# Optimization experiments

Hardware: AMD Instinct MI355X
Metric: run time of the kernel (lower is better)

The kernel has to match this reference:

```python
import jax, jax.numpy as jnp
import numpy as np

HIDDEN = 4096
NUM_HEADS = 32
NUM_KV_HEADS = 8
HEAD_DIM = HIDDEN // NUM_HEADS  # 128
ROPE_THETA = 10000.0
T = 2048


def setup_inputs() -> dict:
    key = jax.random.key(0)
    k1, k2, k3 = jax.random.split(key, 3)
    positions = jnp.arange(T, dtype=jnp.int32)
    hidden_states = jax.random.normal(k1, (T, HIDDEN), dtype=jnp.float32)
    # 0.02 init scale keeps logits in a sane range
    Wqkv = jax.random.normal(k2, (HIDDEN, (NUM_HEADS + 2 * NUM_KV_HEADS) * HEAD_DIM), dtype=jnp.float32) * 0.02
    Wo = jax.random.normal(k3, (HIDDEN, HIDDEN), dtype=jnp.float32) * 0.02
    return {"positions": positions, "hidden_states": hidden_states, "Wqkv": Wqkv, "Wo": Wo}


def _rope_neox(x, positions):
    # x: [T, H, D]; neox style rotates halves of the head dim
    d2 = HEAD_DIM // 2
    inv_freq = ROPE_THETA ** (-jnp.arange(0, d2, dtype=jnp.float32) / d2)
    ang = positions.astype(jnp.float32)[:, None] * inv_freq  # [T, d2]
    cos = jnp.cos(ang)[:, None, :]  # [T,1,d2]
    sin = jnp.sin(ang)[:, None, :]
    x1, x2 = x[..., :d2], x[..., d2:]
    return jnp.concatenate([x1 * cos - x2 * sin, x2 * cos + x1 * sin], axis=-1)


def reference(positions, hidden_states, Wqkv, Wo):
    Tn = hidden_states.shape[0]
    q_sz = NUM_HEADS * HEAD_DIM
    kv_sz = NUM_KV_HEADS * HEAD_DIM
    qkv = hidden_states @ Wqkv  # [T, q_sz + 2*kv_sz]
    q = qkv[:, :q_sz].reshape(Tn, NUM_HEADS, HEAD_DIM)
    k = qkv[:, q_sz:q_sz + kv_sz].reshape(Tn, NUM_KV_HEADS, HEAD_DIM)
    v = qkv[:, q_sz + kv_sz:].reshape(Tn, NUM_KV_HEADS, HEAD_DIM)
    q = _rope_neox(q, positions)
    k = _rope_neox(k, positions)
    # GQA: repeat kv heads to match q heads
    rep = NUM_HEADS // NUM_KV_HEADS
    k = jnp.repeat(k, rep, axis=1)  # [T, H, D]
    v = jnp.repeat(v, rep, axis=1)
    scale = HEAD_DIM ** -0.5
    scores = jnp.einsum('thd,shd->hts', q, k) * scale  # [H, T, T]
    causal = positions[:, None] >= positions[None, :]  # [T, T]
    scores = jnp.where(causal[None, :, :], scores, jnp.float32(-1e30))
    probs = jax.nn.softmax(scores, axis=-1)
    attn = jnp.einsum('hts,shd->thd', probs, v).reshape(Tn, HIDDEN)
    return attn @ Wo
```

## Files before the change

### kernel.cpp

```cpp
#include <hip/hip_runtime.h>
#include <hip/hip_bf16.h>
#include <math.h>

#define T_SEQ 2048
#define HID   4096
#define NH    32
#define NKV   8
#define HD    128
#define QKVD  6144
#define KOFF  4096
#define VOFF  5120

typedef unsigned short u16;
typedef unsigned int   u32;
typedef __attribute__((ext_vector_type(4))) float f32x4;
typedef __attribute__((ext_vector_type(8))) short s16x8;
typedef __attribute__((ext_vector_type(4))) unsigned short u16x4;

__device__ inline u16 f2bf(float f) {
  u32 u = __float_as_uint(f);
  u32 r = u + 0x7FFFu + ((u >> 16) & 1u);
  return (u16)(r >> 16);
}
__device__ inline float bf2f(u16 h) { return __uint_as_float(((u32)h) << 16); }

__device__ inline void gl_lds16(const void* g, void* l) {
  __builtin_amdgcn_global_load_lds((const __attribute__((address_space(1))) void*)g,
                                   (__attribute__((address_space(3))) void*)l, 16, 0, 0);
}

__global__ void cast_f32_bf16(const float* __restrict__ in, u16* __restrict__ out, int n) {
  int i = (blockIdx.x * blockDim.x + threadIdx.x) * 4;
  if (i < n) {
    float4 v = *(const float4*)(in + i);
    u16x4 o = { f2bf(v.x), f2bf(v.y), f2bf(v.z), f2bf(v.w) };
    *(u16x4*)(out + i) = o;
  }
}

__global__ void transpose_cast(const float* __restrict__ in, u16* __restrict__ out, int K, int N) {
  __shared__ float tile[32][33];
  int n0 = blockIdx.x * 32, k0 = blockIdx.y * 32;
  int tx = threadIdx.x, ty = threadIdx.y;
  for (int i = ty; i < 32; i += 8)
    tile[i][tx] = in[(size_t)(k0 + i) * N + n0 + tx];
  __syncthreads();
  for (int i = ty; i < 32; i += 8)
    out[(size_t)(n0 + i) * K + k0 + tx] = f2bf(tile[tx][i]);
}

__global__ void vtrans(const u16* __restrict__ qkv, u16* __restrict__ Vt) {
  __shared__ u16 tile[32][33];
  int kv = blockIdx.z;
  int t0 = blockIdx.x * 32, d0 = blockIdx.y * 32;
  int tx = threadIdx.x, ty = threadIdx.y;
  for (int i = ty; i < 32; i += 8)
    tile[i][tx] = qkv[(size_t)(t0 + i) * QKVD + VOFF + kv * HD + d0 + tx];
  __syncthreads();
  for (int i = ty; i < 32; i += 8)
    Vt[(size_t)(kv * HD + d0 + i) * T_SEQ + t0 + tx] = tile[tx][i];
}

__global__ void rope_kernel(u16* __restrict__ qkv, const int* __restrict__ positions) {
  int t = blockIdx.x;
  int h = blockIdx.y * 4 + (threadIdx.x >> 6);
  int i = threadIdx.x & 63;
  float pos = (float)positions[t];
  float freq = exp2f(-(float)i * (13.287712379549449f / 64.0f));
  float ang = pos * freq;
  float s, c;
  sincosf(ang, &s, &c);
  size_t off;
  if (h < NH) off = (size_t)t * QKVD + h * HD;
  else        off = (size_t)t * QKVD + KOFF + (h - NH) * HD;
  float x1 = bf2f(qkv[off + i]);
  float x2 = bf2f(qkv[off + 64 + i]);
  qkv[off + i]      = f2bf(x1 * c - x2 * s);
  qkv[off + 64 + i] = f2bf(x2 * c + x1 * s);
}

__device__ inline void stage_unit(const u16* __restrict__ G, int K, u16* lds, int w, int l) {
  const int rl = l >> 3;
  const int row = 8 * w + rl;
  const int cs = ((l & 7) ^ rl) << 3;
  gl_lds16(G + (size_t)row * K + cs, lds + 8 * w * 64);
}

#define RD(base, row) (*(const s16x8*)((base) + (size_t)(row) * 64 + ((((kk) * 4 + lg) ^ xsw) << 3)))
#define MM(i, j) acc[i][j] = __builtin_amdgcn_mfma_f32_16x16x32_bf16(a[i][kk], b[j][kk], acc[i][j], 0, 0, 0)

__global__ __launch_bounds__(512, 2) void gemm_qkv(const u16* __restrict__ A, const u16* __restrict__ B,
                                                   u16* __restrict__ C, int M, int N, int K) {
  __shared__ __align__(16) u16 As[2][256 * 64];
  __shared__ __align__(16) u16 Bs[2][192 * 64];
  const int tid = threadIdx.x;
  const int w = tid >> 6, l = tid & 63;
  const int lr = l & 15, lg = l >> 4;
  const int wm = w >> 2, wn = w & 3;
  const int xsw = lr & 7;
  const int bm = blockIdx.y * 256, bn = blockIdx.x * 192;
  const int NT = K >> 6;

  f32x4 acc[8][3] = {};
  s16x8 a[8][2], b[3][2];

#pragma unroll
  for (int u = 0; u < 4; u++) stage_unit(A + (size_t)(bm + 64 * u) * K, K, As[0] + u * 4096, w, l);
#pragma unroll
  for (int u = 0; u < 3; u++) stage_unit(B + (size_t)(bn + 64 * u) * K, K, Bs[0] + u * 4096, w, l);
#pragma unroll
  for (int u = 0; u < 4; u++) stage_unit(A + (size_t)(bm + 64 * u) * K + 64, K, As[1] + u * 4096, w, l);
  asm volatile("s_waitcnt vmcnt(4)" ::: "memory");
  __builtin_amdgcn_s_barrier();

  for (int t = 0; t < NT; t++) {
    const int cur = t & 1;
    const u16* Ah = As[cur];
    const u16* Bh = Bs[cur];
    const int k1 = (t + 1) * 64, k2 = (t + 2) * 64;

#pragma unroll
    for (int kk = 0; kk < 2; kk++) {
#pragma unroll
      for (int i = 0; i < 4; i++) a[i][kk] = RD(Ah, wm * 128 + i * 16 + lr);
#pragma unroll
      for (int j = 0; j < 2; j++) b[j][kk] = RD(Bh, wn * 48 + j * 16 + lr);
    }
    if (t + 1 < NT) {
      stage_unit(B + (size_t)(bn) * K + k1, K, Bs[cur ^ 1] + 0 * 4096, w, l);
      stage_unit(B + (size_t)(bn + 64) * K + k1, K, Bs[cur ^ 1] + 1 * 4096, w, l);
    }
    __builtin_amdgcn_s_barrier();
    asm volatile("s_waitcnt lgkmcnt(0)" ::: "memory");
    __builtin_amdgcn_sched_barrier(0);
    __builtin_amdgcn_s_setprio(1);
#pragma unroll
    for (int kk = 0; kk < 2; kk++)
#pragma unroll
      for (int i = 0; i < 4; i++) { MM(i, 0); MM(i, 1); }
    __builtin_amdgcn_s_setprio(0);
    __builtin_amdgcn_s_barrier();

#pragma unroll
    for (int kk = 0; kk < 2; kk++) {
#pragma unroll
      for (int i = 4; i < 8; i++) a[i][kk] = RD(Ah, wm * 128 + i * 16 + lr);
      b[2][kk] = RD(Bh, wn * 48 + 2 * 16 + lr);
    }
    if (t + 1 < NT)
      stage_unit(B + (size_t)(bn + 128) * K + k1, K, Bs[cur ^ 1] + 2 * 4096, w, l);
    __builtin_amdgcn_s_barrier();
    asm volatile("s_waitcnt lgkmcnt(0)" ::: "memory");
    __builtin_amdgcn_sched_barrier(0);
    __builtin_amdgcn_s_setprio(1);
#pragma unroll
    for (int kk = 0; kk < 2; kk++)
#pragma unroll
      for (int i = 0; i < 8; i++) MM(i, 2);
    __builtin_amdgcn_s_setprio(0);
    __builtin_amdgcn_s_barrier();

    if (t + 2 < NT) {
      stage_unit(A + (size_t)(bm) * K + k2, K, As[cur] + 0 * 4096, w, l);
      stage_unit(A + (size_t)(bm + 64) * K + k2, K, As[cur] + 1 * 4096, w, l);
    }
    __builtin_amdgcn_s_barrier();
    __builtin_amdgcn_s_setprio(1);
#pragma unroll
    for (int kk = 0; kk < 2; kk++)
#pragma unroll
      for (int i = 4; i < 8; i++) MM(i, 0);
    __builtin_amdgcn_s_setprio(0);
    __builtin_amdgcn_s_barrier();

    if (t + 2 < NT) {
      stage_unit(A + (size_t)(bm + 128) * K + k2, K, As[cur] + 2 * 4096, w, l);
      stage_unit(A + (size_t)(bm + 192) * K + k2, K, As[cur] + 3 * 4096, w, l);
      asm volatile("s_waitcnt vmcnt(4)" ::: "memory");
    } else {
      asm volatile("s_waitcnt vmcnt(0)" ::: "memory");
    }
    __builtin_amdgcn_s_barrier();
    __builtin_amdgcn_s_setprio(1);
#pragma unroll
    for (int kk = 0; kk < 2; kk++)
#pragma unroll
      for (int i = 4; i < 8; i++) MM(i, 1);
    __builtin_amdgcn_s_setprio(0);
    __builtin_amdgcn_s_barrier();
  }

#pragma unroll
  for (int i = 0; i < 8; i++)
#pragma unroll
    for (int j = 0; j < 3; j++)
#pragma unroll
      for (int r = 0; r < 4; r++) {
        int row = bm + wm * 128 + i * 16 + lg * 4 + r;
        int col = bn + wn * 48 + j * 16 + lr;
        C[(size_t)row * N + col] = f2bf(acc[i][j][r]);
      }
}

__global__ __launch_bounds__(512, 2) void gemm_out(const u16* __restrict__ A, const u16* __restrict__ B,
                                                   float* __restrict__ C, int M, int N, int K) {
  __shared__ __align__(16) u16 As3[3 * 128 * 64];
  __shared__ __align__(16) u16 Bs3[3 * 256 * 64];
  const int tid = threadIdx.x;
  const int w = tid >> 6, l = tid & 63;
  const int lr = l & 15, lg = l >> 4;
  const int wm = w >> 2, wn = w & 3;
  const int xsw = lr & 7;
  const int bm = blockIdx.y * 128, bn = blockIdx.x * 256;
  const int NT = K >> 6;

  f32x4 acc[4][4] = {};
  s16x8 a[4][2], b[4][2];

#pragma unroll
  for (int u = 0; u < 2; u++) stage_unit(A + (size_t)(bm + 64 * u) * K, K, As3 + u * 4096, w, l);
#pragma unroll
  for (int u = 0; u < 4; u++) stage_unit(B + (size_t)(bn + 64 * u) * K, K, Bs3 + u * 4096, w, l);
#pragma unroll
  for (int u = 0; u < 2; u++) stage_unit(A + (size_t)(bm + 64 * u) * K + 64, K, As3 + 8192 + u * 4096, w, l);
#pragma unroll
  for (int u = 0; u < 4; u++) stage_unit(B + (size_t)(bn + 64 * u) * K + 64, K, Bs3 + 16384 + u * 4096, w, l);
  asm volatile("s_waitcnt vmcnt(6)" ::: "memory");
  __builtin_amdgcn_s_barrier();

  int cur = 0;
  for (int t = 0; t < NT; t++) {
    const u16* Ah = As3 + cur * 8192;
    const u16* Bh = Bs3 + cur * 16384;
    int sb = cur + 2; if (sb >= 3) sb -= 3;
    u16* Asb = As3 + sb * 8192;
    u16* Bsb = Bs3 + sb * 16384;
    const int k2 = (t + 2) * 64;

#pragma unroll
    for (int kk = 0; kk < 2; kk++) {
#pragma unroll
      for (int i = 0; i < 4; i++) a[i][kk] = RD(Ah, wm * 64 + i * 16 + lr);
#pragma unroll
      for (int j = 0; j < 2; j++) b[j][kk] = RD(Bh, wn * 64 + j * 16 + lr);
    }
    if (t + 2 < NT) {
      stage_unit(B + (size_t)(bn) * K + k2, K, Bsb + 0 * 4096, w, l);
      stage_unit(B + (size_t)(bn + 64) * K + k2, K, Bsb + 1 * 4096, w, l);
      stage_unit(B + (size_t)(bn + 128) * K + k2, K, Bsb + 2 * 4096, w, l);
    }
    __builtin_amdgcn_s_barrier();
    asm volatile("s_waitcnt lgkmcnt(0)" ::: "memory");
    __builtin_amdgcn_sched_barrier(0);
    __builtin_amdgcn_s_setprio(1);
#pragma unroll
    for (int kk = 0; kk < 2; kk++)
#pragma unroll
      for (int i = 0; i < 4; i++) { MM(i, 0); MM(i, 1); }
    __builtin_amdgcn_s_setprio(0);
    __builtin_amdgcn_s_barrier();

#pragma unroll
    for (int kk = 0; kk < 2; kk++)
#pragma unroll
      for (int j = 2; j < 4; j++) b[j][kk] = RD(Bh, wn * 64 + j * 16 + lr);
    if (t + 2 < NT) {
      stage_unit(B + (size_t)(bn + 192) * K + k2, K, Bsb + 3 * 4096, w, l);
      stage_unit(A + (size_t)(bm) * K + k2, K, Asb + 0 * 4096, w, l);
      stage_unit(A + (size_t)(bm + 64) * K + k2, K, Asb + 1 * 4096, w, l);
      asm volatile("s_waitcnt vmcnt(6)" ::: "memory");
    } else {
      asm volatile("s_waitcnt vmcnt(0)" ::: "memory");
    }
    __builtin_amdgcn_s_barrier();
    asm volatile("s_waitcnt lgkmcnt(0)" ::: "memory");
    __builtin_amdgcn_sched_barrier(0);
    __builtin_amdgcn_s_setprio(1);
#pragma unroll
    for (int kk = 0; kk < 2; kk++)
#pragma unroll
      for (int i = 0; i < 4; i++) { MM(i, 2); MM(i, 3); }
    __builtin_amdgcn_s_setprio(0);
    __builtin_amdgcn_s_barrier();

    cur = (cur == 2) ? 0 : cur + 1;
  }

#pragma unroll
  for (int i = 0; i < 4; i++)
#pragma unroll
    for (int j = 0; j < 4; j++)
#pragma unroll
      for (int r = 0; r < 4; r++) {
        int row = bm + wm * 64 + i * 16 + lg * 4 + r;
        int col = bn + wn * 64 + j * 16 + lr;
        C[(size_t)row * N + col] = acc[i][j][r];
      }
}
#undef RD
#undef MM

__device__ inline void stage_tiles(const u16* __restrict__ qkv, const u16* __restrict__ Vt,
                                   u16* Kb, u16* Vb, int kv0, int hkv, int w, int l) {
  const int krow_l = l >> 4;
  const int kcb = (l & 15) << 4;
  const int vrow_l = l >> 3;
  const int vcb = (l & 7) << 4;
#pragma unroll
  for (int c = 0; c < 4; c++) {
    int row = c * 16 + w * 4 + krow_l;
    const char* src = (const char*)(qkv + (size_t)(kv0 + row) * QKVD + KOFF + hkv * HD) +
                      (kcb ^ ((row & 7) << 4));
    gl_lds16(src, (char*)Kb + (c * 16 + w * 4) * 256);
  }
#pragma unroll
  for (int c = 0; c < 4; c++) {
    int row = c * 32 + w * 8 + vrow_l;
    const char* src = (const char*)(Vt + (size_t)(hkv * HD + row) * T_SEQ + kv0) +
                      (vcb ^ ((row & 7) << 4));
    gl_lds16(src, (char*)Vb + (c * 32 + w * 8) * 128);
  }
}

__global__ __launch_bounds__(256) void attn_fwd(const u16* __restrict__ qkv, const u16* __restrict__ Vt,
                                                u16* __restrict__ attnout) {
  __shared__ __align__(16) u16 Ks[2][64 * 128];
  __shared__ __align__(16) u16 Vs[2][128 * 64];
  __shared__ __align__(16) u16 plds[4][16 * 72];
  const int tid = threadIdx.x;
  const int w = tid >> 6, l = tid & 63;
  const int lr = l & 15, g = l >> 4;
  const int h = blockIdx.y;
  const int hkv = h >> 2;
  const int swzl = (lr & 7) << 4;
  const float scale = 0.08838834764831845f;
  u16* pw = &plds[w][0];

  for (int seg = 0; seg < 2; seg++) {
    const int qt = (seg == 0) ? blockIdx.x : (31 - blockIdx.x);
    const int q0 = qt * 64 + w * 16;
    const int q_abs = q0 + lr;

    s16x8 qf[4];
    const u16* qbase = qkv + (size_t)(q0 + lr) * QKVD + h * HD + g * 8;
#pragma unroll
    for (int kk = 0; kk < 4; kk++) qf[kk] = *(const s16x8*)(qbase + kk * 32);

    f32x4 acc_o[8] = {};
    float m_run = -__builtin_inff();
    float l_run = 0.0f;
    const int nt = qt + 1;

    stage_tiles(qkv, Vt, Ks[0], Vs[0], 0, hkv, w, l);
    asm volatile("s_waitcnt vmcnt(0)" ::: "memory");
    __syncthreads();
    int cur = 0;
    for (int kt = 0; kt < nt; kt++) {
      const int kv0 = kt * 64;
      if (kt + 1 < nt)
        stage_tiles(qkv, Vt, Ks[cur ^ 1], Vs[cur ^ 1], kv0 + 64, hkv, w, l);
      const bool masked = (kt == qt);

      f32x4 sa[4];
      const char* kb = (const char*)Ks[cur];
#pragma unroll
      for (int ct = 0; ct < 4; ct++) {
        f32x4 aa = {0.f, 0.f, 0.f, 0.f};
#pragma unroll
        for (int kk = 0; kk < 4; kk++) {
          s16x8 kf = *(const s16x8*)(kb + (ct * 16 + lr) * 256 + (((kk << 6) + (g << 4)) ^ swzl));
          aa = __builtin_amdgcn_mfma_f32_16x16x32_bf16(kf, qf[kk], aa, 0, 0, 0);
        }
        sa[ct] = aa;
      }

      float p[16];
      float pmax = -__builtin_inff();
#pragma unroll
      for (int ct = 0; ct < 4; ct++)
#pragma unroll
        for (int r = 0; r < 4; r++) {
          float s = sa[ct][r] * scale;
          if (masked) {
            int kv_abs = kv0 + ct * 16 + g * 4 + r;
            if (kv_abs > q_abs) s = -__builtin_inff();
          }
          p[ct * 4 + r] = s;
          pmax = fmaxf(pmax, s);
        }
      pmax = fmaxf(pmax, __shfl_xor(pmax, 16, 64));
      pmax = fmaxf(pmax, __shfl_xor(pmax, 32, 64));
      float m_new = fmaxf(m_run, pmax);
      float fac = __expf(m_run - m_new);
      float psum = 0.f;
#pragma unroll
      for (int x = 0; x < 16; x++) {
        float e = __expf(p[x] - m_new);
        p[x] = e;
        psum += e;
      }
      psum += __shfl_xor(psum, 16, 64);
      psum += __shfl_xor(psum, 32, 64);
      l_run = l_run * fac + psum;
      m_run = m_new;
      float fr[4];
#pragma unroll
      for (int r = 0; r < 4; r++) fr[r] = __shfl(fac, g * 4 + r, 64);
#pragma unroll
      for (int dt = 0; dt < 8; dt++)
#pragma unroll
        for (int r = 0; r < 4; r++) acc_o[dt][r] *= fr[r];

#pragma unroll
      for (int ct = 0; ct < 4; ct++) {
        u16x4 pk = { f2bf(p[ct * 4 + 0]), f2bf(p[ct * 4 + 1]), f2bf(p[ct * 4 + 2]), f2bf(p[ct * 4 + 3]) };
        *(u16x4*)(pw + lr * 72 + ct * 16 + g * 4) = pk;
      }
      asm volatile("s_waitcnt lgkmcnt(0)" ::: "memory");
      __builtin_amdgcn_sched_barrier(0);
      s16x8 pa0 = *(const s16x8*)(pw + lr * 72 + g * 8);
      s16x8 pa1 = *(const s16x8*)(pw + lr * 72 + 32 + g * 8);

      const char* vbb = (const char*)Vs[cur];
#pragma unroll
      for (int dt = 0; dt < 8; dt++) {
        s16x8 v0 = *(const s16x8*)(vbb + (dt * 16 + lr) * 128 + ((g << 4) ^ swzl));
        s16x8 v1 = *(const s16x8*)(vbb + (dt * 16 + lr) * 128 + ((64 + (g << 4)) ^ swzl));
        acc_o[dt] = __builtin_amdgcn_mfma_f32_16x16x32_bf16(pa0, v0, acc_o[dt], 0, 0, 0);
        acc_o[dt] = __builtin_amdgcn_mfma_f32_16x16x32_bf16(pa1, v1, acc_o[dt], 0, 0, 0);
      }
      asm volatile("s_waitcnt vmcnt(0)" ::: "memory");
      __syncthreads();
      cur ^= 1;
    }

    float ln[4];
#pragma unroll
    for (int r = 0; r < 4; r++) ln[r] = __shfl(l_run, g * 4 + r, 64);
#pragma unroll
    for (int dt = 0; dt < 8; dt++)
#pragma unroll
      for (int r = 0; r < 4; r++) {
        int row = q0 + g * 4 + r;
        int col = h * HD + dt * 16 + lr;
        attnout[(size_t)row * HID + col] = f2bf(acc_o[dt][r] / ln[r]);
      }
  }
}

extern "C" void kernel_launch(void* const* d_in, const int* in_sizes, int n_in,
                              void* d_out, int out_size, void* d_ws, size_t ws_size,
                              hipStream_t stream) {
  const int*   positions = (const int*)d_in[0];
  const float* X         = (const float*)d_in[1];
  const float* Wqkv      = (const float*)d_in[2];
  const float* Wo        = (const float*)d_in[3];
  float* out = (float*)d_out;

  char* ws = (char*)d_ws;
  size_t off = 0;
  u16* Xbf    = (u16*)(ws + off); off += (size_t)T_SEQ * HID * 2;
  u16* Wqkvt  = (u16*)(ws + off); off += (size_t)QKVD * HID * 2;
  u16* Wot    = (u16*)(ws + off); off += (size_t)HID * HID * 2;
  u16* qkv    = (u16*)(ws + off); off += (size_t)T_SEQ * QKVD * 2;
  u16* Vt     = (u16*)(ws + off); off += (size_t)NKV * HD * T_SEQ * 2;
  u16* attnb  = (u16*)(ws + off); off += (size_t)T_SEQ * HID * 2;

  cast_f32_bf16<<<dim3((T_SEQ * HID) / (256 * 4)), dim3(256), 0, stream>>>(X, Xbf, T_SEQ * HID);
  transpose_cast<<<dim3(QKVD / 32, HID / 32), dim3(32, 8), 0, stream>>>(Wqkv, Wqkvt, HID, QKVD);
  transpose_cast<<<dim3(HID / 32, HID / 32), dim3(32, 8), 0, stream>>>(Wo, Wot, HID, HID);
  gemm_qkv<<<dim3(QKVD / 192, T_SEQ / 256), dim3(512), 0, stream>>>(Xbf, Wqkvt, qkv, T_SEQ, QKVD, HID);
  rope_kernel<<<dim3(T_SEQ, 10), dim3(256), 0, stream>>>(qkv, positions);
  vtrans<<<dim3(T_SEQ / 32, HD / 32, NKV), dim3(32, 8), 0, stream>>>(qkv, Vt);
  attn_fwd<<<dim3(16, 32), dim3(256), 0, stream>>>(qkv, Vt, attnb);
  gemm_out<<<dim3(HID / 256, T_SEQ / 128), dim3(512), 0, stream>>>(attnb, Wot, out, T_SEQ, HID, HID);
}
```

Before: 536.5 us.

## Rewrite attention with 32x32 MFMA, 512-thread blocks, and lazy softmax rescale

The attention kernel now uses 32x32x16 bf16 MFMA with 8 waves per block. Each wave handles 32 query rows, and the two halves of the block process a complementary pair of 128-row query tiles while sharing staged K/V tiles. P is kept in registers via packed bf16 conversion, with the V^T column order permuted in vtrans so the MFMA layouts line up; this removes the LDS round-trip for probabilities. The online softmax skips the rescale unless the row max grows by more than a threshold. The intent is higher MFMA throughput and fewer LDS and ALU operations per tile, at the cost of higher register pressure and some idle waves on tiles they do not need.

Result: faster. 521.9 us (-2.7%).

```diff
diff --git a/kernel.cpp b/kernel.cpp
--- a/kernel.cpp
+++ b/kernel.cpp
@@ -14,6 +14,7 @@
 typedef unsigned short u16;
 typedef unsigned int   u32;
 typedef __attribute__((ext_vector_type(4))) float f32x4;
+typedef __attribute__((ext_vector_type(16))) float f32x16;
 typedef __attribute__((ext_vector_type(8))) short s16x8;
 typedef __attribute__((ext_vector_type(4))) unsigned short u16x4;
 
@@ -27,6 +28,12 @@
 __device__ inline void gl_lds16(const void* g, void* l) {
   __builtin_amdgcn_global_load_lds((const __attribute__((address_space(1))) void*)g,
                                    (__attribute__((address_space(3))) void*)l, 16, 0, 0);
+}
+
+__device__ inline u32 cvtpk_bf16(float a, float b) {
+  u32 r;
+  asm("v_cvt_pk_bf16_f32 %0, %1, %2" : "=v"(r) : "v"(a), "v"(b));
+  return r;
 }
 
 __global__ void cast_f32_bf16(const float* __restrict__ in, u16* __restrict__ out, int n) {
@@ -57,8 +64,9 @@
   for (int i = ty; i < 32; i += 8)
     tile[i][tx] = qkv[(size_t)(t0 + i) * QKVD + VOFF + kv * HD + d0 + tx];
   __syncthreads();
+  int txp = (tx & 16) | (tx & 3) | ((tx & 4) << 1) | ((tx & 8) >> 1);
   for (int i = ty; i < 32; i += 8)
-    Vt[(size_t)(kv * HD + d0 + i) * T_SEQ + t0 + tx] = tile[tx][i];
+    Vt[(size_t)(kv * HD + d0 + i) * T_SEQ + t0 + txp] = tile[tx][i];
 }
 
 __global__ void rope_kernel(u16* __restrict__ qkv, const int* __restrict__ positions) {
@@ -81,9 +89,8 @@
 
 __device__ inline void stage_unit(const u16* __restrict__ G, int K, u16* lds, int w, int l) {
   const int rl = l >> 3;
-  const int row = 8 * w + rl;
   const int cs = ((l & 7) ^ rl) << 3;
-  gl_lds16(G + (size_t)row * K + cs, lds + 8 * w * 64);
+  gl_lds16(G + (size_t)(8 * w + rl) * K + cs, lds + 8 * w * 64);
 }
 
 #define RD(base, row) (*(const s16x8*)((base) + (size_t)(row) * 64 + ((((kk) * 4 + lg) ^ xsw) << 3)))
@@ -300,151 +307,129 @@
 #undef RD
 #undef MM
 
-__device__ inline void stage_tiles(const u16* __restrict__ qkv, const u16* __restrict__ Vt,
-                                   u16* Kb, u16* Vb, int kv0, int hkv, int w, int l) {
-  const int krow_l = l >> 4;
-  const int kcb = (l & 15) << 4;
-  const int vrow_l = l >> 3;
-  const int vcb = (l & 7) << 4;
-#pragma unroll
-  for (int c = 0; c < 4; c++) {
-    int row = c * 16 + w * 4 + krow_l;
+__device__ inline void stage_kv8(const u16* __restrict__ qkv, const u16* __restrict__ Vt,
+                                 char* Kb, char* Vb, int kv0, int hkv, int w, int l) {
+  const int c16 = l & 15, r16 = l >> 4;
+  const int c8 = l & 7, r8 = l >> 3;
+#pragma unroll
+  for (int i = 0; i < 2; i++) {
+    int row = i * 32 + w * 4 + r16;
     const char* src = (const char*)(qkv + (size_t)(kv0 + row) * QKVD + KOFF + hkv * HD) +
-                      (kcb ^ ((row & 7) << 4));
-    gl_lds16(src, (char*)Kb + (c * 16 + w * 4) * 256);
-  }
-#pragma unroll
-  for (int c = 0; c < 4; c++) {
-    int row = c * 32 + w * 8 + vrow_l;
-    const char* src = (const char*)(Vt + (size_t)(hkv * HD + row) * T_SEQ + kv0) +
-                      (vcb ^ ((row & 7) << 4));
-    gl_lds16(src, (char*)Vb + (c * 32 + w * 8) * 128);
-  }
-}
-
-__global__ __launch_bounds__(256) void attn_fwd(const u16* __restrict__ qkv, const u16* __restrict__ Vt,
-                                                u16* __restrict__ attnout) {
-  __shared__ __align__(16) u16 Ks[2][64 * 128];
-  __shared__ __align__(16) u16 Vs[2][128 * 64];
-  __shared__ __align__(16) u16 plds[4][16 * 72];
+                      ((c16 ^ (row & 7)) << 4);
+    gl_lds16(src, Kb + i * 8192 + w * 1024);
+  }
+#pragma unroll
+  for (int i = 0; i < 2; i++) {
+    int drow = i * 64 + w * 8 + r8;
+    const char* src = (const char*)(Vt + (size_t)(hkv * HD + drow) * T_SEQ + kv0) +
+                      ((c8 ^ (drow & 7)) << 4);
+    gl_lds16(src, Vb + i * 8192 + w * 1024);
+  }
+}
+
+__global__ __launch_bounds__(512, 2) void attn_fwd(const u16* __restrict__ qkv, const u16* __restrict__ Vt,
+                                                   u16* __restrict__ attnout) {
+  __shared__ __align__(16) char Ks[2][64 * 256];
+  __shared__ __align__(16) char Vs[2][128 * 128];
   const int tid = threadIdx.x;
   const int w = tid >> 6, l = tid & 63;
-  const int lr = l & 15, g = l >> 4;
-  const int h = blockIdx.y;
-  const int hkv = h >> 2;
-  const int swzl = (lr & 7) << 4;
+  const int l31 = l & 31, hi = l >> 5, l7 = l & 7;
+  const int h = blockIdx.y, hkv = h >> 2;
+  const int x = blockIdx.x;
+  const int qt = (w < 4) ? (15 - x) : x;
+  const int q0 = qt * 128 + (w & 3) * 32;
+  const int my_nt = 2 * qt + 2;
+  const int NT = 32 - 2 * x;
+  const int q_abs = q0 + l31;
   const float scale = 0.08838834764831845f;
-  u16* pw = &plds[w][0];
-
-  for (int seg = 0; seg < 2; seg++) {
-    const int qt = (seg == 0) ? blockIdx.x : (31 - blockIdx.x);
-    const int q0 = qt * 64 + w * 16;
-    const int q_abs = q0 + lr;
-
-    s16x8 qf[4];
-    const u16* qbase = qkv + (size_t)(q0 + lr) * QKVD + h * HD + g * 8;
-#pragma unroll
-    for (int kk = 0; kk < 4; kk++) qf[kk] = *(const s16x8*)(qbase + kk * 32);
-
-    f32x4 acc_o[8] = {};
-    float m_run = -__builtin_inff();
-    float l_run = 0.0f;
-    const int nt = qt + 1;
-
-    stage_tiles(qkv, Vt, Ks[0], Vs[0], 0, hkv, w, l);
+
+  s16x8 qf[8];
+  const u16* qb = qkv + (size_t)q_abs * QKVD + h * HD + hi * 8;
+#pragma unroll
+  for (int dk = 0; dk < 8; dk++) qf[dk] = *(const s16x8*)(qb + dk * 16);
+
+  f32x16 acc[4] = {};
+  float m_run = -1e30f, l_run = 0.0f;
+
+  stage_kv8(qkv, Vt, Ks[0], Vs[0], 0, hkv, w, l);
+  asm volatile("s_waitcnt vmcnt(0)" ::: "memory");
+  __syncthreads();
+  int cur = 0;
+  for (int kt = 0; kt < NT; kt++) {
+    if (kt + 1 < NT)
+      stage_kv8(qkv, Vt, Ks[cur ^ 1], Vs[cur ^ 1], (kt + 1) * 64, hkv, w, l);
+    if (kt < my_nt) {
+      const char* kb = Ks[cur];
+      f32x16 s0 = {}, s1 = {};
+#pragma unroll
+      for (int dk = 0; dk < 8; dk++) {
+        int cs = (((dk << 1) + hi) ^ l7) << 4;
+        s16x8 k0 = *(const s16x8*)(kb + l31 * 256 + cs);
+        s16x8 k1 = *(const s16x8*)(kb + (32 + l31) * 256 + cs);
+        s0 = __builtin_amdgcn_mfma_f32_32x32x16_bf16(k0, qf[dk], s0, 0, 0, 0);
+        s1 = __builtin_amdgcn_mfma_f32_32x32x16_bf16(k1, qf[dk], s1, 0, 0, 0);
+      }
+      const bool masked = (kt >= my_nt - 2);
+      float ps[32];
+      float pmax = -1e30f;
+#pragma unroll
+      for (int r = 0; r < 16; r++) {
+        float v0 = s0[r] * scale, v1 = s1[r] * scale;
+        if (masked) {
+          int kvo = kt * 64 + (r & 3) + 8 * (r >> 2) + 4 * hi;
+          if (kvo > q_abs) v0 = -1e30f;
+          if (kvo + 32 > q_abs) v1 = -1e30f;
+        }
+        ps[r] = v0; ps[16 + r] = v1;
+        pmax = fmaxf(pmax, fmaxf(v0, v1));
+      }
+      pmax = fmaxf(pmax, __shfl_xor(pmax, 32, 64));
+      if (!__all(pmax <= m_run + 8.0f)) {
+        float m_new = fmaxf(m_run, pmax);
+        float fac = __expf(m_run - m_new);
+        l_run *= fac;
+#pragma unroll
+        for (int r = 0; r < 16; r++) {
+          float fr = __shfl(fac, (r & 3) + 8 * (r >> 2) + 4 * hi, 64);
+#pragma unroll
+          for (int db = 0; db < 4; db++) acc[db][r] *= fr;
+        }
+        m_run = m_new;
+      }
+      float psum = 0.f;
+#pragma unroll
+      for (int i = 0; i < 32; i++) { float e = __expf(ps[i] - m_run); ps[i] = e; psum += e; }
+      psum += __shfl_xor(psum, 32, 64);
+      l_run += psum;
+      s16x8 pf[4];
+#pragma unroll
+      for (int ks = 0; ks < 4; ks++) {
+        union { u32 uw[4]; s16x8 v; } u;
+#pragma unroll
+        for (int q = 0; q < 4; q++) u.uw[q] = cvtpk_bf16(ps[8 * ks + 2 * q], ps[8 * ks + 2 * q + 1]);
+        pf[ks] = u.v;
+      }
+      const char* vb = Vs[cur];
+#pragma unroll
+      for (int db = 0; db < 4; db++)
+#pragma unroll
+        for (int ks = 0; ks < 4; ks++) {
+          s16x8 vf = *(const s16x8*)(vb + (db * 32 + l31) * 128 + ((((ks << 1) + hi) ^ l7) << 4));
+          acc[db] = __builtin_amdgcn_mfma_f32_32x32x16_bf16(pf[ks], vf, acc[db], 0, 0, 0);
+        }
+    }
     asm volatile("s_waitcnt vmcnt(0)" ::: "memory");
     __syncthreads();
-    int cur = 0;
-    for (int kt = 0; kt < nt; kt++) {
-      const int kv0 = kt * 64;
-      if (kt + 1 < nt)
-        stage_tiles(qkv, Vt, Ks[cur ^ 1], Vs[cur ^ 1], kv0 + 64, hkv, w, l);
-      const bool masked = (kt == qt);
-
-      f32x4 sa[4];
-      const char* kb = (const char*)Ks[cur];
-#pragma unroll
-      for (int ct = 0; ct < 4; ct++) {
-        f32x4 aa = {0.f, 0.f, 0.f, 0.f};
-#pragma unroll
-        for (int kk = 0; kk < 4; kk++) {
-          s16x8 kf = *(const s16x8*)(kb + (ct * 16 + lr) * 256 + (((kk << 6) + (g << 4)) ^ swzl));
-          aa = __builtin_amdgcn_mfma_f32_16x16x32_bf16(kf, qf[kk], aa, 0, 0, 0);
-        }
-        sa[ct] = aa;
-      }
-
-      float p[16];
-      float pmax = -__builtin_inff();
-#pragma unroll
-      for (int ct = 0; ct < 4; ct++)
-#pragma unroll
-        for (int r = 0; r < 4; r++) {
-          float s = sa[ct][r] * scale;
-          if (masked) {
-            int kv_abs = kv0 + ct * 16 + g * 4 + r;
-            if (kv_abs > q_abs) s = -__builtin_inff();
-          }
-          p[ct * 4 + r] = s;
-          pmax = fmaxf(pmax, s);
-        }
-      pmax = fmaxf(pmax, __shfl_xor(pmax, 16, 64));
-      pmax = fmaxf(pmax, __shfl_xor(pmax, 32, 64));
-      float m_new = fmaxf(m_run, pmax);
-      float fac = __expf(m_run - m_new);
-      float psum = 0.f;
-#pragma unroll
-      for (int x = 0; x < 16; x++) {
-        float e = __expf(p[x] - m_new);
-        p[x] = e;
-        psum += e;
-      }
-      psum += __shfl_xor(psum, 16, 64);
-      psum += __shfl_xor(psum, 32, 64);
-      l_run = l_run * fac + psum;
-      m_run = m_new;
-      float fr[4];
-#pragma unroll
-      for (int r = 0; r < 4; r++) fr[r] = __shfl(fac, g * 4 + r, 64);
-#pragma unroll
-      for (int dt = 0; dt < 8; dt++)
-#pragma unroll
-        for (int r = 0; r < 4; r++) acc_o[dt][r] *= fr[r];
-
-#pragma unroll
-      for (int ct = 0; ct < 4; ct++) {
-        u16x4 pk = { f2bf(p[ct * 4 + 0]), f2bf(p[ct * 4 + 1]), f2bf(p[ct * 4 + 2]), f2bf(p[ct * 4 + 3]) };
-        *(u16x4*)(pw + lr * 72 + ct * 16 + g * 4) = pk;
-      }
-      asm volatile("s_waitcnt lgkmcnt(0)" ::: "memory");
-      __builtin_amdgcn_sched_barrier(0);
-      s16x8 pa0 = *(const s16x8*)(pw + lr * 72 + g * 8);
-      s16x8 pa1 = *(const s16x8*)(pw + lr * 72 + 32 + g * 8);
-
-      const char* vbb = (const char*)Vs[cur];
-#pragma unroll
-      for (int dt = 0; dt < 8; dt++) {
-        s16x8 v0 = *(const s16x8*)(vbb + (dt * 16 + lr) * 128 + ((g << 4) ^ swzl));
-        s16x8 v1 = *(const s16x8*)(vbb + (dt * 16 + lr) * 128 + ((64 + (g << 4)) ^ swzl));
-        acc_o[dt] = __builtin_amdgcn_mfma_f32_16x16x32_bf16(pa0, v0, acc_o[dt], 0, 0, 0);
-        acc_o[dt] = __builtin_amdgcn_mfma_f32_16x16x32_bf16(pa1, v1, acc_o[dt], 0, 0, 0);
-      }
-      asm volatile("s_waitcnt vmcnt(0)" ::: "memory");
-      __syncthreads();
-      cur ^= 1;
-    }
-
-    float ln[4];
-#pragma unroll
-    for (int r = 0; r < 4; r++) ln[r] = __shfl(l_run, g * 4 + r, 64);
-#pragma unroll
-    for (int dt = 0; dt < 8; dt++)
-#pragma unroll
-      for (int r = 0; r < 4; r++) {
-        int row = q0 + g * 4 + r;
-        int col = h * HD + dt * 16 + lr;
-        attnout[(size_t)row * HID + col] = f2bf(acc_o[dt][r] / ln[r]);
-      }
+    cur ^= 1;
+  }
+#pragma unroll
+  for (int r = 0; r < 16; r++) {
+    int cr = (r & 3) + 8 * (r >> 2) + 4 * hi;
+    float ln = __shfl(l_run, cr, 64);
+    float inv = 1.0f / ln;
+    u16* ob = attnout + (size_t)(q0 + cr) * HID + h * HD + l31;
+#pragma unroll
+    for (int db = 0; db < 4; db++) ob[db * 32] = f2bf(acc[db][r] * inv);
   }
 }
 
@@ -472,6 +457,6 @@
   gemm_qkv<<<dim3(QKVD / 192, T_SEQ / 256), dim3(512), 0, stream>>>(Xbf, Wqkvt, qkv, T_SEQ, QKVD, HID);
   rope_kernel<<<dim3(T_SEQ, 10), dim3(256), 0, stream>>>(qkv, positions);
   vtrans<<<dim3(T_SEQ / 32, HD / 32, NKV), dim3(32, 8), 0, stream>>>(qkv, Vt);
-  attn_fwd<<<dim3(16, 32), dim3(256), 0, stream>>>(qkv, Vt, attnb);
+  attn_fwd<<<dim3(8, 32), dim3(512), 0, stream>>>(qkv, Vt, attnb);
   gemm_out<<<dim3(HID / 256, T_SEQ / 128), dim3(512), 0, stream>>>(attnb, Wot, out, T_SEQ, HID, HID);
 }
```
